# Kernel tuning notes

Measured on AMD Instinct MI355X. Metric: run time of the kernel, lower is better.

## Reference

```python
import jax, jax.numpy as jnp
import numpy as np

B, S, D, H = 2, 2048, 1024, 16
DK = D // H  # 64
ROPE_THETA = 10000.0


def apply_rope(t, positions):
    # t: [B, H, S, DK]; positions: [B, S]
    half = DK // 2
    inv_freq = 1.0 / (ROPE_THETA ** (jnp.arange(0, DK, 2, dtype=jnp.float32) / DK))  # [half]
    ang = positions.astype(jnp.float32)[:, None, :, None] * inv_freq  # [B,1,S,half]
    cos, sin = jnp.cos(ang), jnp.sin(ang)
    t_even = t[..., 0::2]
    t_odd = t[..., 1::2]
    r_even = t_even * cos - t_odd * sin
    r_odd = t_even * sin + t_odd * cos
    # interleave back to original layout
    return jnp.stack([r_even, r_odd], axis=-1).reshape(t.shape)


def setup_inputs() -> dict:
    key = jax.random.key(0)
    ks = jax.random.split(key, 5)
    x = jax.random.normal(ks[0], (B, S, D), dtype=jnp.float32)
    token_positions = jnp.broadcast_to(jnp.arange(S, dtype=jnp.int64 if jax.config.jax_enable_x64 else jnp.int32), (B, S))
    w_q = jax.random.normal(ks[1], (D, D), dtype=jnp.float32)
    w_k = jax.random.normal(ks[2], (D, D), dtype=jnp.float32)
    w_v = jax.random.normal(ks[3], (D, D), dtype=jnp.float32)
    w_o = jax.random.normal(ks[4], (D, D), dtype=jnp.float32)
    return {"x": x, "token_positions": token_positions, "w_q": w_q, "w_k": w_k, "w_v": w_v, "w_o": w_o}


def reference(x, token_positions, w_q, w_k, w_v, w_o):
    # project: weights stored as (h*d_k, d_model)
    wq = w_q.reshape(H, DK, D)
    wk = w_k.reshape(H, DK, D)
    wv = w_v.reshape(H, DK, D)
    q = jnp.einsum('bsd,hkd->bhsk', x, wq)  # [B,H,S,DK]
    k = jnp.einsum('bsd,hkd->bhsk', x, wk)
    v = jnp.einsum('bsd,hkd->bhsk', x, wv)
    q = apply_rope(q, token_positions)
    k = apply_rope(k, token_positions)
    scale = 1.0 / jnp.sqrt(jnp.float32(DK))
    scores = jnp.einsum('bhnk,bhmk->bhnm', q, k) * scale  # [B,H,S,S]
    causal = jnp.tril(jnp.ones((S, S), dtype=bool))
    scores = jnp.where(causal, scores, -jnp.inf)
    attn = jax.nn.softmax(scores, axis=-1)
    out = jnp.einsum('bhnm,bhmv->bhnv', attn, v)  # [B,H,S,DK]
    out = jnp.transpose(out, (0, 2, 1, 3)).reshape(B, S, H * DK)
    return jnp.einsum('bsf,df->bsd', out, w_o)
```

## Files before the change

### kernel.cpp

```cpp
#include <hip/hip_runtime.h>

typedef unsigned short u16;
typedef unsigned int u32;
typedef __attribute__((ext_vector_type(8))) __bf16 bf16x8;
typedef __attribute__((ext_vector_type(4))) float f32x4;

#define NSEQ 2048
#define NDIM 1024
#define NHEAD 16
#define NTOK 4096
#define NX   4194304
#define NWEL 1048576

__device__ __forceinline__ u16 f2bf(float f) {
  unsigned u = __float_as_uint(f);
  return (u16)((u + 0x7fffu + ((u >> 16) & 1u)) >> 16);
}
__device__ __forceinline__ float bf2f(u16 h) {
  return __uint_as_float(((unsigned)h) << 16);
}
__device__ __forceinline__ bf16x8 ld16(const u16* p) {
  int4 v = *reinterpret_cast<const int4*>(p);
  return __builtin_bit_cast(bf16x8, v);
}
__device__ __forceinline__ f32x4 mfma16(bf16x8 a, bf16x8 b, f32x4 c) {
  return __builtin_amdgcn_mfma_f32_16x16x32_bf16(a, b, c, 0, 0, 0);
}
__device__ __forceinline__ u32 cvtpk(float lo, float hi) {
  u32 r;
  asm("v_cvt_pk_bf16_f32 %0, %1, %2" : "=v"(r) : "v"(lo), "v"(hi));
  return r;
}
__device__ __forceinline__ float max3f(float a, float b, float c) {
  float d;
  asm("v_max3_f32 %0, %1, %2, %3" : "=v"(d) : "v"(a), "v"(b), "v"(c));
  return d;
}
__device__ __forceinline__ void gload16(const u16* g, u16* l) {
  __builtin_amdgcn_global_load_lds(
      (const __attribute__((address_space(1))) void*)g,
      (__attribute__((address_space(3))) void*)l, 16, 0, 0);
}

#define GEMM_PROLOGUE                                                         \
  const int tid = threadIdx.x;                                                \
  const int lane = tid & 63, wid = tid >> 6;                                  \
  const int wm = wid >> 1, wn = wid & 1;                                      \
  const int lr = lane & 15, lg = lane >> 4;                                   \
  const int srow_ = tid >> 2;                                                 \
  const int sch_ = ((tid & 3) ^ ((tid >> 3) & 3)) * 8;                        \
  const int rsw_ = (lg ^ ((lr >> 1) & 3)) * 8;

#define STAGE3(BB, AH, AL, BH, BL, T0, J0, K0)                                \
  {                                                                           \
    u16* bb_ = (BB);                                                          \
    gload16(AH + (size_t)((T0) + srow_) * NDIM + (K0) + sch_, bb_ + tid * 8); \
    gload16(AH + (size_t)((T0) + 64 + srow_) * NDIM + (K0) + sch_,            \
            bb_ + 2048 + tid * 8);                                            \
    gload16(BH + (size_t)((J0) + srow_) * NDIM + (K0) + sch_,                 \
            bb_ + 4096 + tid * 8);                                            \
    gload16(BH + (size_t)((J0) + 64 + srow_) * NDIM + (K0) + sch_,            \
            bb_ + 6144 + tid * 8);                                            \
    gload16(AL + (size_t)((T0) + srow_) * NDIM + (K0) + sch_,                 \
            bb_ + 8192 + tid * 8);                                            \
    gload16(AL + (size_t)((T0) + 64 + srow_) * NDIM + (K0) + sch_,            \
            bb_ + 10240 + tid * 8);                                           \
    gload16(BL + (size_t)((J0) + srow_) * NDIM + (K0) + sch_,                 \
            bb_ + 12288 + tid * 8);                                           \
    gload16(BL + (size_t)((J0) + 64 + srow_) * NDIM + (K0) + sch_,            \
            bb_ + 14336 + tid * 8);                                           \
  }

#define GEMM3_LOOP(AH, AL, BH, BL, T0, J0)                                    \
  STAGE3(lds, AH, AL, BH, BL, T0, J0, 0)                                      \
  __syncthreads();                                                            \
  for (int k0 = 0; k0 < NDIM; k0 += 32) {                                     \
    u16* cb_ = lds + ((k0 >> 5) & 1) * 16384;                                 \
    if (k0 + 32 < NDIM) {                                                     \
      u16* nb_ = lds + ((((k0 >> 5) & 1) ^ 1) * 16384);                       \
      STAGE3(nb_, AH, AL, BH, BL, T0, J0, k0 + 32)                            \
    }                                                                         \
    bf16x8 afh[4], afl[4];                                                    \
    _Pragma("unroll") for (int m = 0; m < 4; m++) {                           \
      int off = (wm * 64 + m * 16 + lr) * 32 + rsw_;                          \
      afh[m] = ld16(cb_ + off);                                               \
      afl[m] = ld16(cb_ + 8192 + off);                                        \
    }                                                                         \
    _Pragma("unroll") for (int n = 0; n < 4; n++) {                           \
      int off = (wn * 64 + n * 16 + lr) * 32 + rsw_;                          \
      bf16x8 bfh = ld16(cb_ + 4096 + off);                                    \
      bf16x8 bfl = ld16(cb_ + 12288 + off);                                   \
      _Pragma("unroll") for (int m = 0; m < 4; m++) {                         \
        acc[m][n] = mfma16(afh[m], bfh, acc[m][n]);                           \
        acc[m][n] = mfma16(afh[m], bfl, acc[m][n]);                           \
        acc[m][n] = mfma16(afl[m], bfh, acc[m][n]);                           \
      }                                                                       \
    }                                                                         \
    __syncthreads();                                                          \
  }

#define STAGE1(BB, AH, BH, T0, J0, K0)                                        \
  {                                                                           \
    u16* bb_ = (BB);                                                          \
    gload16(AH + (size_t)((T0) + srow_) * NDIM + (K0) + sch_, bb_ + tid * 8); \
    gload16(AH + (size_t)((T0) + 64 + srow_) * NDIM + (K0) + sch_,            \
            bb_ + 2048 + tid * 8);                                            \
    gload16(BH + (size_t)((J0) + srow_) * NDIM + (K0) + sch_,                 \
            bb_ + 4096 + tid * 8);                                            \
    gload16(BH + (size_t)((J0) + 64 + srow_) * NDIM + (K0) + sch_,            \
            bb_ + 6144 + tid * 8);                                            \
  }

#define GEMM1_LOOP(AH, BH, T0, J0)                                            \
  STAGE1(lds, AH, BH, T0, J0, 0)                                              \
  __syncthreads();                                                            \
  for (int k0 = 0; k0 < NDIM; k0 += 32) {                                     \
    u16* cb_ = lds + ((k0 >> 5) & 1) * 8192;                                  \
    if (k0 + 32 < NDIM) {                                                     \
      u16* nb_ = lds + ((((k0 >> 5) & 1) ^ 1) * 8192);                        \
      STAGE1(nb_, AH, BH, T0, J0, k0 + 32)                                    \
    }                                                                         \
    bf16x8 afh[4];                                                            \
    _Pragma("unroll") for (int m = 0; m < 4; m++) {                           \
      int off = (wm * 64 + m * 16 + lr) * 32 + rsw_;                          \
      afh[m] = ld16(cb_ + off);                                               \
    }                                                                         \
    _Pragma("unroll") for (int n = 0; n < 4; n++) {                           \
      int off = (wn * 64 + n * 16 + lr) * 32 + rsw_;                          \
      bf16x8 bfh = ld16(cb_ + 4096 + off);                                    \
      _Pragma("unroll") for (int m = 0; m < 4; m++) {                         \
        acc[m][n] = mfma16(afh[m], bfh, acc[m][n]);                           \
      }                                                                       \
    }                                                                         \
    __syncthreads();                                                          \
  }

__global__ __launch_bounds__(256) void k_prep(
    const float* __restrict__ x, const float* __restrict__ wq,
    const float* __restrict__ wk, const float* __restrict__ wv,
    const float* __restrict__ wo,
    u16* __restrict__ xh, u16* __restrict__ xl,
    u16* __restrict__ wh, u16* __restrict__ wl,
    float2* __restrict__ csn) {
  if (blockIdx.x >= 8192) {
    int idx = (blockIdx.x - 8192) * 256 + threadIdx.x;
    int p = idx >> 5, j = idx & 31;
    double invf = exp((double)(2 * j) * (-9.210340371976184 / 64.0));
    double ang = (double)p * invf;
    double kq = rint(ang * 0.15915494309189535);
    float a = (float)(ang - kq * 6.283185307179586);
    csn[idx] = make_float2(cosf(a), sinf(a));
    return;
  }
  int g = blockIdx.x * 256 + threadIdx.x;
  const float4* src;
  u16 *dh, *dl;
  int idx;
  bool wantlo = true;
  if (g < NX / 4) {
    src = (const float4*)x; dh = xh; dl = xl; idx = g;
  } else {
    int z = (g - NX / 4) / (NWEL / 4);
    int r = (g - NX / 4) % (NWEL / 4);
    src = (const float4*)(z == 0 ? wq : z == 1 ? wk : z == 2 ? wv : wo);
    dh = wh + (size_t)z * NWEL; dl = wl + (size_t)z * NWEL; idx = r;
    wantlo = (z < 2);
  }
  float4 v = src[idx];
  u16 h0 = f2bf(v.x), h1 = f2bf(v.y), h2 = f2bf(v.z), h3 = f2bf(v.w);
  ushort4 hv = make_ushort4(h0, h1, h2, h3);
  ((ushort4*)dh)[idx] = hv;
  if (wantlo) {
    ushort4 lv = make_ushort4(f2bf(v.x - bf2f(h0)), f2bf(v.y - bf2f(h1)),
                              f2bf(v.z - bf2f(h2)), f2bf(v.w - bf2f(h3)));
    ((ushort4*)dl)[idx] = lv;
  }
}

__global__ __launch_bounds__(256) void k_qkv(
    const u16* __restrict__ xh, const u16* __restrict__ xl,
    const u16* __restrict__ wh, const u16* __restrict__ wl,
    const int* __restrict__ tokpos, const float2* __restrict__ csn,
    u16* __restrict__ qh, u16* __restrict__ ql,
    u16* __restrict__ kh, u16* __restrict__ kl, u16* __restrict__ vt) {
  __shared__ __align__(16) u16 lds[32768];
  const int z = blockIdx.z;
  const int t0 = blockIdx.y * 128, j0 = blockIdx.x * 128;
  const int h0 = j0 >> 6;
  GEMM_PROLOGUE
  f32x4 acc[4][4];
#pragma unroll
  for (int m = 0; m < 4; m++)
#pragma unroll
    for (int n = 0; n < 4; n++) acc[m][n] = f32x4{0.f, 0.f, 0.f, 0.f};
  const int b = t0 >> 11, s0 = t0 & 2047;

  if (z == 2) {
    const u16* wvh = wh + 2 * (size_t)NWEL;
    GEMM1_LOOP(xh, wvh, t0, j0)
#pragma unroll
    for (int m = 0; m < 4; m++)
#pragma unroll
      for (int r = 0; r < 4; r++) {
        int rloc = wm * 64 + m * 16 + lg * 4 + r;
#pragma unroll
        for (int n = 0; n < 4; n++) {
          int cloc = wn * 64 + n * 16 + lr;
          lds[cloc * 128 + (rloc ^ ((cloc & 15) << 3))] = f2bf(acc[m][n][r]);
        }
      }
    __syncthreads();
#pragma unroll
    for (int i = 0; i < 8; i++) {
      int idx = tid + i * 256;
      int col = idx >> 4, rc = idx & 15;
      int4 v = *(int4*)(lds + col * 128 + ((rc * 8) ^ ((col & 15) << 3)));
      int h2 = col >> 6, dk = col & 63;
      size_t off =
          ((size_t)((b * NHEAD + h0 + h2) * 64 + dk)) * NSEQ + s0 + rc * 8;
      *(int4*)(vt + off) = v;
    }
    return;
  }

  const u16* Bh = wh + (size_t)z * NWEL;
  const u16* Bl = wl + (size_t)z * NWEL;
  GEMM3_LOOP(xh, xl, Bh, Bl, t0, j0)

  u16* dh = (z == 0) ? qh : kh;
  u16* dl = (z == 0) ? ql : kl;
  const float scl = (z == 0) ? 0.18033688011112042f : 1.0f;
#pragma unroll
  for (int m = 0; m < 4; m++) {
#pragma unroll
    for (int r = 0; r < 4; r++) {
      int pos = tokpos[t0 + wm * 64 + m * 16 + lg * 4 + r];
      int rloc = wm * 64 + m * 16 + lg * 4 + r;
#pragma unroll
      for (int n = 0; n < 4; n++) {
        float val = acc[m][n][r];
        float nb = __shfl_xor(val, 1);
        int dk = (wn * 64 + n * 16 + lr) & 63;
        float2 cs = csn[pos * 32 + (dk >> 1)];
        float v = ((dk & 1) ? (nb * cs.y + val * cs.x)
                            : (val * cs.x - nb * cs.y)) * scl;
        int cloc = wn * 64 + n * 16 + lr;
        u16 hi = f2bf(v);
        lds[rloc * 128 + cloc] = hi;
        lds[16384 + rloc * 128 + cloc] = f2bf(v - bf2f(hi));
      }
    }
  }
  __syncthreads();
#pragma unroll
  for (int i = 0; i < 16; i++) {
    int idx = tid + i * 256;
    int plane = idx >> 11, i2 = idx & 2047;
    int r = i2 >> 4, cc = i2 & 15;
    int4 v = *(int4*)(lds + plane * 16384 + r * 128 + cc * 8);
    int h2 = cc >> 3, dk = (cc & 7) * 8;
    u16* dst = plane ? dl : dh;
    size_t off = ((size_t)((b * NHEAD + h0 + h2) * NSEQ + s0 + r)) * 64 + dk;
    *(int4*)(dst + off) = v;
  }
}

#define ATT_STAGE(SEL)                                                        \
  _Pragma("unroll") for (int j_ = 0; j_ < 3; j_++) {                          \
    gload16(asrc[j_], adst[j_] + (SEL) * 4096);                               \
    asrc[j_] += astr[j_];                                                     \
  }

__global__ __launch_bounds__(512) void k_attn(
    const u16* __restrict__ qh, const u16* __restrict__ ql,
    const u16* __restrict__ kh, const u16* __restrict__ kl,
    const u16* __restrict__ vt, u16* __restrict__ ah) {
  __shared__ __align__(16) u16 skh[2][4096];
  __shared__ __align__(16) u16 skl[2][4096];
  __shared__ __align__(16) u16 svb[2][4096];
  __shared__ __align__(16) u16 sp[8192];
  const int tid = threadIdx.x, lane = tid & 63, w = tid >> 6;
  const int lr = lane & 15, lg = lane >> 4;
  const int fid = blockIdx.y * 16 + blockIdx.x;
  const int xcd = fid & 7, j = fid >> 3;
  const int rank = j >> 2, lbh = j & 3;
  const int bh = xcd * 4 + lbh;
  const int qt = 15 - rank;
  const size_t base = (size_t)bh * NSEQ * 64;
  const size_t vbase = (size_t)bh * 64 * NSEQ;
  const int b = bh >> 4, h = bh & 15;
  const int q0 = qt * 128;
  const int nt = 2 * qt + 2;

  const int qrow_g = q0 + w * 16 + lr;
  bf16x8 qfh[2], qfl[2];
#pragma unroll
  for (int kk = 0; kk < 2; kk++) {
    qfh[kk] = ld16(qh + base + (size_t)qrow_g * 64 + kk * 32 + lg * 8);
    qfl[kk] = ld16(ql + base + (size_t)qrow_g * 64 + kk * 32 + lg * 8);
  }
  float mrun = -__builtin_inff(), lrun = 0.f;
  f32x4 oacc[4];
#pragma unroll
  for (int nf = 0; nf < 4; nf++) oacc[nf] = f32x4{0.f, 0.f, 0.f, 0.f};

  const u16* asrc[3];
  u16* adst[3];
  int astr[3];
#pragma unroll
  for (int j_ = 0; j_ < 3; j_++) {
    int seg_ = w * 3 + j_;
    int ten_ = seg_ >> 3, sub_ = seg_ & 7;
    int row_ = sub_ * 8 + (lane >> 3);
    int sc_ = ((lane & 7) * 8) ^ ((row_ & 7) * 8);
    adst[j_] = (ten_ == 0 ? &skh[0][0] : ten_ == 1 ? &skl[0][0] : &svb[0][0]) +
               sub_ * 512;
    astr[j_] = (ten_ == 2) ? 64 : 4096;
    asrc[j_] = (ten_ == 2)
                   ? vt + vbase + (size_t)row_ * NSEQ + sc_
                   : (ten_ == 0 ? kh : kl) + base + (size_t)row_ * 64 + sc_;
  }

  int sel = 0;
  ATT_STAGE(0)
  __syncthreads();
  for (int kt = 0; kt < nt; kt++) {
    if (kt + 1 < nt) { ATT_STAGE(sel ^ 1) }
    f32x4 sacc[4];
#pragma unroll
    for (int nf = 0; nf < 4; nf++) sacc[nf] = f32x4{0.f, 0.f, 0.f, 0.f};
    __builtin_amdgcn_s_setprio(1);
#pragma unroll
    for (int nf = 0; nf < 4; nf++) {
      int krow = nf * 16 + lr;
      int swz = (krow & 7) * 8;
#pragma unroll
      for (int kk = 0; kk < 2; kk++) {
        int off = krow * 64 + ((kk * 32 + lg * 8) ^ swz);
        bf16x8 kfh = ld16(&skh[sel][0] + off);
        bf16x8 kfl = ld16(&skl[sel][0] + off);
        sacc[nf] = mfma16(kfh, qfh[kk], sacc[nf]);
        sacc[nf] = mfma16(kfl, qfh[kk], sacc[nf]);
        sacc[nf] = mfma16(kfh, qfl[kk], sacc[nf]);
      }
    }
    __builtin_amdgcn_s_setprio(0);
    float sv[4][4], mm[4];
#pragma unroll
    for (int nf = 0; nf < 4; nf++) {
#pragma unroll
      for (int r = 0; r < 4; r++) sv[nf][r] = sacc[nf][r];
    }
    if (kt >= nt - 2) {
#pragma unroll
      for (int nf = 0; nf < 4; nf++)
#pragma unroll
        for (int r = 0; r < 4; r++) {
          int colg = kt * 64 + nf * 16 + lg * 4 + r;
          if (colg > qrow_g) sv[nf][r] = -__builtin_inff();
        }
    }
#pragma unroll
    for (int nf = 0; nf < 4; nf++)
      mm[nf] = fmaxf(max3f(sv[nf][0], sv[nf][1], sv[nf][2]), sv[nf][3]);
    float rmax = fmaxf(max3f(mm[0], mm[1], mm[2]), mm[3]);
    rmax = fmaxf(rmax, __shfl_xor(rmax, 16));
    rmax = fmaxf(rmax, __shfl_xor(rmax, 32));
    float alpha = 1.f;
    bool resc = __any(rmax > mrun + 8.f);
    if (resc) {
      float mnew = fmaxf(mrun, rmax);
      alpha = exp2f(mrun - mnew);
      mrun = mnew;
      lrun *= alpha;
    }
    float p[4][4];
    float ss[4];
#pragma unroll
    for (int nf = 0; nf < 4; nf++) {
#pragma unroll
      for (int r = 0; r < 4; r++) p[nf][r] = exp2f(sv[nf][r] - mrun);
      ss[nf] = (p[nf][0] + p[nf][1]) + (p[nf][2] + p[nf][3]);
    }
    float rsum = (ss[0] + ss[1]) + (ss[2] + ss[3]);
    rsum += __shfl_xor(rsum, 16);
    rsum += __shfl_xor(rsum, 32);
    lrun += rsum;
    {
      int prow = w * 16 + lr;
      int swz = (prow & 7) * 8;
#pragma unroll
      for (int nf = 0; nf < 4; nf++) {
        u32 w0 = cvtpk(p[nf][0], p[nf][1]);
        u32 w1 = cvtpk(p[nf][2], p[nf][3]);
        int col = (nf * 16 + lg * 4) ^ swz;
        *(uint2*)(&sp[prow * 64 + col]) = make_uint2(w0, w1);
      }
    }
    if (resc) {
      float af0 = __shfl(alpha, lg * 4 + 0);
      float af1 = __shfl(alpha, lg * 4 + 1);
      float af2 = __shfl(alpha, lg * 4 + 2);
      float af3 = __shfl(alpha, lg * 4 + 3);
#pragma unroll
      for (int nf = 0; nf < 4; nf++) {
        oacc[nf][0] *= af0; oacc[nf][1] *= af1;
        oacc[nf][2] *= af2; oacc[nf][3] *= af3;
      }
    }
    {
      int prow = w * 16 + lr;
      int pswz = (prow & 7) * 8;
      __builtin_amdgcn_s_setprio(1);
#pragma unroll
      for (int kk = 0; kk < 2; kk++) {
        bf16x8 pa = ld16(&sp[prow * 64 + ((kk * 32 + lg * 8) ^ pswz)]);
#pragma unroll
        for (int nf = 0; nf < 4; nf++) {
          int vrow = nf * 16 + lr;
          bf16x8 vb2 = ld16(&svb[sel][0] + vrow * 64 +
                            ((kk * 32 + lg * 8) ^ ((vrow & 7) * 8)));
          oacc[nf] = mfma16(pa, vb2, oacc[nf]);
        }
      }
      __builtin_amdgcn_s_setprio(0);
    }
    __syncthreads();
    sel ^= 1;
  }
  float inv = 1.0f / lrun;
  float iv0 = __shfl(inv, lg * 4 + 0);
  float iv1 = __shfl(inv, lg * 4 + 1);
  float iv2 = __shfl(inv, lg * 4 + 2);
  float iv3 = __shfl(inv, lg * 4 + 3);
#pragma unroll
  for (int r = 0; r < 4; r++) {
    float ivr = r == 0 ? iv0 : r == 1 ? iv1 : r == 2 ? iv2 : iv3;
    int row = q0 + w * 16 + lg * 4 + r;
    size_t toff = ((size_t)(b * NSEQ + row)) * NDIM + h * 64;
#pragma unroll
    for (int nf = 0; nf < 4; nf++) {
      ah[toff + nf * 16 + lr] = f2bf(oacc[nf][r] * ivr);
    }
  }
}

__global__ __launch_bounds__(256) void k_out(
    const u16* __restrict__ ah, const u16* __restrict__ wh,
    float* __restrict__ out) {
  __shared__ __align__(16) u16 lds[16384];
  const int t0 = blockIdx.y * 128, j0 = blockIdx.x * 128;
  GEMM_PROLOGUE
  f32x4 acc[4][4];
#pragma unroll
  for (int m = 0; m < 4; m++)
#pragma unroll
    for (int n = 0; n < 4; n++) acc[m][n] = f32x4{0.f, 0.f, 0.f, 0.f};
  GEMM1_LOOP(ah, wh, t0, j0)
#pragma unroll
  for (int m = 0; m < 4; m++)
#pragma unroll
    for (int r = 0; r < 4; r++) {
      int row = t0 + wm * 64 + m * 16 + lg * 4 + r;
#pragma unroll
      for (int n = 0; n < 4; n++) {
        int col = j0 + wn * 64 + n * 16 + lr;
        out[(size_t)row * NDIM + col] = acc[m][n][r];
      }
    }
}

extern "C" void kernel_launch(void* const* d_in, const int* in_sizes, int n_in,
                              void* d_out, int out_size, void* d_ws, size_t ws_size,
                              hipStream_t stream) {
  (void)in_sizes; (void)n_in; (void)out_size; (void)ws_size;
  const float* x = (const float*)d_in[0];
  const int* tokpos = (const int*)d_in[1];
  const float* wq = (const float*)d_in[2];
  const float* wk = (const float*)d_in[3];
  const float* wv = (const float*)d_in[4];
  const float* wo = (const float*)d_in[5];
  float* out = (float*)d_out;

  u16* ws = (u16*)d_ws;
  u16* xh = ws;
  u16* xl = xh + NX;
  u16* wh = xl + NX;
  u16* wl = wh + 4 * (size_t)NWEL;
  u16* qh = wl + 4 * (size_t)NWEL;
  u16* ql = qh + NX;
  u16* kh = ql + NX;
  u16* kl = kh + NX;
  u16* vt = kl + NX;
  float2* csn = (float2*)(vt + NX);

  k_prep<<<dim3(8448), dim3(256), 0, stream>>>(x, wq, wk, wv, wo, xh, xl, wh,
                                               wl, csn);
  k_qkv<<<dim3(8, 32, 3), dim3(256), 0, stream>>>(xh, xl, wh, wl, tokpos, csn,
                                                  qh, ql, kh, kl, vt);
  k_attn<<<dim3(16, 32), dim3(512), 0, stream>>>(qh, ql, kh, kl, vt, xh);
  k_out<<<dim3(8, 32), dim3(256), 0, stream>>>(xh, wh + 3 * (size_t)NWEL, out);
}
```

Measured before the change: 168.2 us.

## Halve QKV kernel LDS with single-buffered GEMM and two-pass epilogue

The split-precision Q/K projection loop changes from double-buffered to single-buffered LDS staging, with a barrier before and after each stage. The RoPE epilogue now keeps rotated values in registers and writes the hi and lo bf16 planes through LDS in two sequential passes. Together these halve the shared memory per block so more blocks can be resident per CU. The cost is that global loads no longer overlap with MFMA work, and the epilogue carries extra barriers and register pressure.

```diff
diff --git a/kernel.cpp b/kernel.cpp
--- a/kernel.cpp
+++ b/kernel.cpp
@@ -71,32 +71,27 @@
             bb_ + 14336 + tid * 8);                                           \
   }
 
-#define GEMM3_LOOP(AH, AL, BH, BL, T0, J0)                                    \
-  STAGE3(lds, AH, AL, BH, BL, T0, J0, 0)                                      \
-  __syncthreads();                                                            \
+#define GEMM3S_LOOP(AH, AL, BH, BL, T0, J0)                                   \
   for (int k0 = 0; k0 < NDIM; k0 += 32) {                                     \
-    u16* cb_ = lds + ((k0 >> 5) & 1) * 16384;                                 \
-    if (k0 + 32 < NDIM) {                                                     \
-      u16* nb_ = lds + ((((k0 >> 5) & 1) ^ 1) * 16384);                       \
-      STAGE3(nb_, AH, AL, BH, BL, T0, J0, k0 + 32)                            \
-    }                                                                         \
+    __syncthreads();                                                          \
+    STAGE3(lds, AH, AL, BH, BL, T0, J0, k0)                                   \
+    __syncthreads();                                                          \
     bf16x8 afh[4], afl[4];                                                    \
     _Pragma("unroll") for (int m = 0; m < 4; m++) {                           \
       int off = (wm * 64 + m * 16 + lr) * 32 + rsw_;                          \
-      afh[m] = ld16(cb_ + off);                                               \
-      afl[m] = ld16(cb_ + 8192 + off);                                        \
+      afh[m] = ld16(lds + off);                                               \
+      afl[m] = ld16(lds + 8192 + off);                                        \
     }                                                                         \
     _Pragma("unroll") for (int n = 0; n < 4; n++) {                           \
       int off = (wn * 64 + n * 16 + lr) * 32 + rsw_;                          \
-      bf16x8 bfh = ld16(cb_ + 4096 + off);                                    \
-      bf16x8 bfl = ld16(cb_ + 12288 + off);                                   \
+      bf16x8 bfh = ld16(lds + 4096 + off);                                    \
+      bf16x8 bfl = ld16(lds + 12288 + off);                                   \
       _Pragma("unroll") for (int m = 0; m < 4; m++) {                         \
         acc[m][n] = mfma16(afh[m], bfh, acc[m][n]);                           \
         acc[m][n] = mfma16(afh[m], bfl, acc[m][n]);                           \
         acc[m][n] = mfma16(afl[m], bfh, acc[m][n]);                           \
       }                                                                       \
     }                                                                         \
-    __syncthreads();                                                          \
   }
 
 #define STAGE1(BB, AH, BH, T0, J0, K0)                                        \
@@ -183,7 +178,7 @@
     const int* __restrict__ tokpos, const float2* __restrict__ csn,
     u16* __restrict__ qh, u16* __restrict__ ql,
     u16* __restrict__ kh, u16* __restrict__ kl, u16* __restrict__ vt) {
-  __shared__ __align__(16) u16 lds[32768];
+  __shared__ __align__(16) u16 lds[16384];
   const int z = blockIdx.z;
   const int t0 = blockIdx.y * 128, j0 = blockIdx.x * 128;
   const int h0 = j0 >> 6;
@@ -225,43 +220,55 @@
 
   const u16* Bh = wh + (size_t)z * NWEL;
   const u16* Bl = wl + (size_t)z * NWEL;
-  GEMM3_LOOP(xh, xl, Bh, Bl, t0, j0)
+  GEMM3S_LOOP(xh, xl, Bh, Bl, t0, j0)
 
   u16* dh = (z == 0) ? qh : kh;
   u16* dl = (z == 0) ? ql : kl;
   const float scl = (z == 0) ? 0.18033688011112042f : 1.0f;
+  float rv[4][4][4];
 #pragma unroll
   for (int m = 0; m < 4; m++) {
 #pragma unroll
     for (int r = 0; r < 4; r++) {
       int pos = tokpos[t0 + wm * 64 + m * 16 + lg * 4 + r];
-      int rloc = wm * 64 + m * 16 + lg * 4 + r;
 #pragma unroll
       for (int n = 0; n < 4; n++) {
         float val = acc[m][n][r];
         float nb = __shfl_xor(val, 1);
         int dk = (wn * 64 + n * 16 + lr) & 63;
         float2 cs = csn[pos * 32 + (dk >> 1)];
-        float v = ((dk & 1) ? (nb * cs.y + val * cs.x)
-                            : (val * cs.x - nb * cs.y)) * scl;
-        int cloc = wn * 64 + n * 16 + lr;
-        u16 hi = f2bf(v);
-        lds[rloc * 128 + cloc] = hi;
-        lds[16384 + rloc * 128 + cloc] = f2bf(v - bf2f(hi));
-      }
-    }
-  }
-  __syncthreads();
-#pragma unroll
-  for (int i = 0; i < 16; i++) {
-    int idx = tid + i * 256;
-    int plane = idx >> 11, i2 = idx & 2047;
-    int r = i2 >> 4, cc = i2 & 15;
-    int4 v = *(int4*)(lds + plane * 16384 + r * 128 + cc * 8);
-    int h2 = cc >> 3, dk = (cc & 7) * 8;
-    u16* dst = plane ? dl : dh;
-    size_t off = ((size_t)((b * NHEAD + h0 + h2) * NSEQ + s0 + r)) * 64 + dk;
-    *(int4*)(dst + off) = v;
+        rv[m][r][n] = ((dk & 1) ? (nb * cs.y + val * cs.x)
+                                : (val * cs.x - nb * cs.y)) * scl;
+      }
+    }
+  }
+#pragma unroll
+  for (int pass = 0; pass < 2; pass++) {
+    __syncthreads();
+#pragma unroll
+    for (int m = 0; m < 4; m++)
+#pragma unroll
+      for (int r = 0; r < 4; r++) {
+        int rloc = wm * 64 + m * 16 + lg * 4 + r;
+#pragma unroll
+        for (int n = 0; n < 4; n++) {
+          int cloc = wn * 64 + n * 16 + lr;
+          float v = rv[m][r][n];
+          u16 hi = f2bf(v);
+          lds[rloc * 128 + cloc] = pass == 0 ? hi : f2bf(v - bf2f(hi));
+        }
+      }
+    __syncthreads();
+    u16* dst = pass == 0 ? dh : dl;
+#pragma unroll
+    for (int i = 0; i < 8; i++) {
+      int idx = tid + i * 256;
+      int r = idx >> 4, cc = idx & 15;
+      int4 v = *(int4*)(lds + r * 128 + cc * 8);
+      int h2 = cc >> 3, dk = (cc & 7) * 8;
+      size_t off = ((size_t)((b * NHEAD + h0 + h2) * NSEQ + s0 + r)) * 64 + dk;
+      *(int4*)(dst + off) = v;
+    }
   }
 }
 
```

Result: slower. 203.8 us (+21.2%).
